# Kernel tuning notes

Hardware: AMD Instinct MI355X
Metric: run time of the kernel (lower is better)

## Reference

```python
import jax, jax.numpy as jnp
import numpy as np

SIGMA = 1.0  # RBF kernel bandwidth (init kwarg)

def setup_inputs() -> dict:
    key = jax.random.key(0)
    ks = jax.random.split(key, 5)
    B, N, D_in, D_emb = 8, 2048, 1024, 512
    scale = 1.0 / np.sqrt(D_in)
    return {
        "x": jax.random.normal(ks[0], (B, N, D_in), jnp.float32),
        "W_mu": jax.random.normal(ks[1], (D_emb, D_in), jnp.float32) * scale,
        "b_mu": jax.random.normal(ks[2], (D_emb,), jnp.float32) * scale,
        "W_logvar": jax.random.normal(ks[3], (D_emb, D_in), jnp.float32) * scale,
        "b_logvar": jax.random.normal(ks[4], (D_emb,), jnp.float32) * scale,
    }

def reference(x, W_mu, b_mu, W_logvar, b_logvar):
    # dual linear heads: (B,N,D_in) -> (B,N,D_emb)
    mu = jnp.einsum('bnd,ed->bne', x, W_mu) + b_mu
    logvar = jnp.einsum('bnd,ed->bne', x, W_logvar) + b_logvar
    sigma = jnp.exp(0.5 * logvar)
    # RBF kernel matrix K(x, x): (B,N,N) via ||xi||^2 + ||xj||^2 - 2 xi.xj
    sq = jnp.sum(x * x, axis=-1)                       # (B,N)
    gram = jnp.einsum('bnd,bmd->bnm', x, x)            # (B,N,N)
    dist = sq[:, :, None] + sq[:, None, :] - 2.0 * gram
    K = jnp.exp(-dist / (2.0 * SIGMA ** 2))            # (B,N,N)
    cov_diag = jnp.diagonal(K, axis1=1, axis2=2)       # (B,N) == exp(0) = 1
    sigma_adjusted = sigma * cov_diag[..., None]       # (B,N,D_emb)
    return (mu, sigma_adjusted)
```

## Files before the change

### kernel.cpp

```cpp
#include <hip/hip_runtime.h>
#include <hip/hip_bf16.h>
#include <math.h>

typedef __bf16 bf16;
typedef __attribute__((ext_vector_type(4))) float f32x4;
typedef __attribute__((ext_vector_type(4))) bf16 bf16x4;
typedef __attribute__((ext_vector_type(8))) bf16 bf16x8;

#define M_TOT 16384
#define K_TOT 1024
#define D_EMB 512
#define NT 32

__global__ __launch_bounds__(256) void cvt_w_img(
    const float* __restrict__ W_mu, const float* __restrict__ W_logvar,
    bf16* __restrict__ img)
{
    const int c  = blockIdx.x * 256 + threadIdx.x;
    const int l  = c & 63;
    const int kt = (c >> 6) & 31;
    const int es = c >> 11;
    const int col = es * 16 + (l & 15);
    const int k0  = kt * 32 + (l >> 4) * 8;
    const float* s = (col < D_EMB) ? (W_mu + (size_t)col * K_TOT + k0)
                                   : (W_logvar + (size_t)(col - D_EMB) * K_TOT + k0);
    f32x4 a = ((const f32x4*)s)[0];
    f32x4 b = ((const f32x4*)s)[1];
    bf16x8 o;
    o[0] = (bf16)a[0]; o[1] = (bf16)a[1]; o[2] = (bf16)a[2]; o[3] = (bf16)a[3];
    o[4] = (bf16)b[0]; o[5] = (bf16)b[1]; o[6] = (bf16)b[2]; o[7] = (bf16)b[3];
    *(bf16x8*)(img + (size_t)c * 8) = o;
}

__global__ __launch_bounds__(512, 1) void gpe_tall3(
    const float* __restrict__ x,
    const bf16* __restrict__ wimg,
    const float* __restrict__ b_mu,
    const float* __restrict__ b_logvar,
    float* __restrict__ out)
{
    __shared__ __align__(16) bf16 Alds[64 * 1024];

    const int tid  = threadIdx.x;
    const int lane = tid & 63;
    const int wc   = tid >> 6;
    const int fr   = lane & 15;
    const int g16  = lane >> 4;
    const int frx  = fr & 7;
    const int bm   = blockIdx.x;

    const int arow = tid >> 3;
    const int sl0  = tid & 7;
    const int rx   = arow & 7;
    const float* __restrict__ Asrc = x + (size_t)(bm * 64 + arow) * K_TOT;

    f32x4 stg[8];
    auto gload = [&](int c) {
#pragma unroll
        for (int j = 0; j < 4; ++j) {
            const int s = c * 32 + sl0 + 8 * j;
            stg[2 * j]     = *(const f32x4*)(Asrc + s * 8);
            stg[2 * j + 1] = *(const f32x4*)(Asrc + s * 8 + 4);
        }
    };
    auto cvtwrite = [&](int c) {
#pragma unroll
        for (int j = 0; j < 4; ++j) {
            const int s = c * 32 + sl0 + 8 * j;
            bf16x8 w;
#pragma unroll
            for (int q = 0; q < 4; ++q) {
                w[q]     = (bf16)stg[2 * j][q];
                w[q + 4] = (bf16)stg[2 * j + 1][q];
            }
            *(bf16x8*)&Alds[arow * 1024 + (s ^ rx) * 8] = w;
        }
    };

    const bf16* __restrict__ bl = wimg + lane * 8;
    bf16x8 bvA[4], bvB[4];
    auto loadB = [&](size_t e0, int t, bf16x8 (&bv)[4]) {
#pragma unroll
        for (int ns = 0; ns < 4; ++ns)
            bv[ns] = *(const bf16x8*)(bl + e0 + (size_t)ns * 16384 + t * 512);
    };

    f32x4 acc[4][4];
#pragma unroll
    for (int m = 0; m < 4; ++m)
#pragma unroll
        for (int n = 0; n < 4; ++n)
            acc[m][n] = (f32x4){0.f, 0.f, 0.f, 0.f};

    const size_t e0p0 = (size_t)(wc * 4) * 16384;
    const size_t e0p1 = (size_t)(32 + wc * 4) * 16384;

#define TILE_BODY(T, E0, BVC)                                                  \
    {                                                                          \
        const int t = (T);                                                     \
        bf16x8 afc[4];                                                         \
        _Pragma("unroll")                                                      \
        for (int m = 0; m < 4; ++m)                                            \
            afc[m] = *(const bf16x8*)&Alds[(m * 16 + fr) * 1024                \
                                           + ((t * 4 + g16) ^ frx) * 8];       \
        __builtin_amdgcn_s_setprio(1);                                         \
        _Pragma("unroll")                                                      \
        for (int ns = 0; ns < 4; ++ns)                                         \
            _Pragma("unroll")                                                  \
            for (int m = 0; m < 4; ++m)                                        \
                acc[m][ns] = __builtin_amdgcn_mfma_f32_16x16x32_bf16(          \
                    afc[m], BVC[ns], acc[m][ns], 0, 0, 0);                     \
        __builtin_amdgcn_s_setprio(0);                                         \
        if (t + 2 < NT) loadB(E0, t + 2, BVC);                                 \
    }

    gload(0);
    for (int c = 0; c < 4; ++c) {
        if (c == 0) asm volatile("s_waitcnt vmcnt(0)" ::: "memory");
        else        asm volatile("s_waitcnt vmcnt(8)" ::: "memory");
        cvtwrite(c);
        if (c < 3) gload(c + 1);
        if (c == 0) { loadB(e0p0, 0, bvA); loadB(e0p0, 1, bvB); }
        asm volatile("s_waitcnt lgkmcnt(0)" ::: "memory");
        __builtin_amdgcn_s_barrier();
#pragma unroll
        for (int tt = 0; tt < 8; tt += 2) {
            TILE_BODY(c * 8 + tt,     e0p0, bvA)
            TILE_BODY(c * 8 + tt + 1, e0p0, bvB)
        }
    }

    loadB(e0p1, 0, bvA);
    loadB(e0p1, 1, bvB);
    {
        float* __restrict__ obase = out;
#pragma unroll
        for (int m = 0; m < 4; ++m) {
            const int row0 = bm * 64 + m * 16 + g16 * 4;
#pragma unroll
            for (int ns = 0; ns < 4; ++ns) {
                const int cl = wc * 64 + ns * 16 + fr;
                const float bvs = b_mu[cl];
#pragma unroll
                for (int j = 0; j < 4; ++j)
                    obase[(size_t)(row0 + j) * D_EMB + cl] = acc[m][ns][j] + bvs;
            }
        }
    }

#pragma unroll
    for (int m = 0; m < 4; ++m)
#pragma unroll
        for (int n = 0; n < 4; ++n)
            acc[m][n] = (f32x4){0.f, 0.f, 0.f, 0.f};

#pragma unroll
    for (int tt = 0; tt < NT; tt += 2) {
        TILE_BODY(tt,     e0p1, bvA)
        TILE_BODY(tt + 1, e0p1, bvB)
    }
#undef TILE_BODY

    {
        float* __restrict__ obase = out + (size_t)M_TOT * D_EMB;
#pragma unroll
        for (int m = 0; m < 4; ++m) {
            const int row0 = bm * 64 + m * 16 + g16 * 4;
#pragma unroll
            for (int ns = 0; ns < 4; ++ns) {
                const int cl = wc * 64 + ns * 16 + fr;
                const float bvs = b_logvar[cl];
#pragma unroll
                for (int j = 0; j < 4; ++j)
                    obase[(size_t)(row0 + j) * D_EMB + cl] =
                        __expf(0.5f * (acc[m][ns][j] + bvs));
            }
        }
    }
}

#define LDS_STRIDE 40
__global__ __launch_bounds__(256) void gpe_gemm_fb(
    const float* __restrict__ x, const float* __restrict__ W_mu,
    const float* __restrict__ b_mu, const float* __restrict__ W_logvar,
    const float* __restrict__ b_logvar, float* __restrict__ out)
{
    __shared__ __align__(16) bf16 As[128][LDS_STRIDE];
    __shared__ __align__(16) bf16 Bs[128][LDS_STRIDE];
    const int tid = threadIdx.x, lane = tid & 63, wid = tid >> 6;
    const int wr = wid >> 1, wcn = wid & 1;
    const int bn = blockIdx.x & 7, bm = blockIdx.x >> 3;
    const int ebase = bn * 128;
    const bool is_mu = (ebase < D_EMB);
    const float* Wp = is_mu ? (W_mu + (size_t)ebase * K_TOT)
                            : (W_logvar + (size_t)(ebase - D_EMB) * K_TOT);
    const float* bias = is_mu ? b_mu : b_logvar;
    const int cbase = is_mu ? ebase : (ebase - D_EMB);
    float* obase = is_mu ? out : (out + (size_t)M_TOT * D_EMB);
    const float* Ap = x + (size_t)(bm * 128) * K_TOT;
    f32x4 acc[4][4];
#pragma unroll
    for (int m = 0; m < 4; ++m)
#pragma unroll
        for (int n = 0; n < 4; ++n) acc[m][n] = (f32x4){0.f, 0.f, 0.f, 0.f};
    const int fr = lane & 15, fk = (lane >> 4) * 8;
    const int arow = wr * 64 + fr, brow = wcn * 64 + fr;
    for (int kt = 0; kt < K_TOT / 32; ++kt) {
        const int k0 = kt * 32;
#pragma unroll
        for (int s = 0; s < 4; ++s) {
            const int idx = s * 256 + tid;
            const int row = idx >> 3, col = (idx & 7) << 2;
            f32x4 va = *reinterpret_cast<const f32x4*>(Ap + (size_t)row * K_TOT + k0 + col);
            f32x4 vb = *reinterpret_cast<const f32x4*>(Wp + (size_t)row * K_TOT + k0 + col);
            bf16x4 ha, hb;
#pragma unroll
            for (int j = 0; j < 4; ++j) { ha[j] = (bf16)va[j]; hb[j] = (bf16)vb[j]; }
            *reinterpret_cast<bf16x4*>(&As[row][col]) = ha;
            *reinterpret_cast<bf16x4*>(&Bs[row][col]) = hb;
        }
        __syncthreads();
        bf16x8 af[4], bfv[4];
#pragma unroll
        for (int m = 0; m < 4; ++m)
            af[m] = *reinterpret_cast<const bf16x8*>(&As[arow + m * 16][fk]);
#pragma unroll
        for (int n = 0; n < 4; ++n)
            bfv[n] = *reinterpret_cast<const bf16x8*>(&Bs[brow + n * 16][fk]);
#pragma unroll
        for (int m = 0; m < 4; ++m)
#pragma unroll
            for (int n = 0; n < 4; ++n)
                acc[m][n] = __builtin_amdgcn_mfma_f32_16x16x32_bf16(af[m], bfv[n], acc[m][n], 0, 0, 0);
        __syncthreads();
    }
#pragma unroll
    for (int m = 0; m < 4; ++m) {
        const int rbase = bm * 128 + wr * 64 + m * 16 + (lane >> 4) * 4;
#pragma unroll
        for (int n = 0; n < 4; ++n) {
            const int c = cbase + wcn * 64 + n * 16 + (lane & 15);
            const float bv = bias[c];
#pragma unroll
            for (int j = 0; j < 4; ++j) {
                float v = acc[m][n][j] + bv;
                if (!is_mu) v = __expf(0.5f * v);
                obase[(size_t)(rbase + j) * D_EMB + c] = v;
            }
        }
    }
}

extern "C" void kernel_launch(void* const* d_in, const int* in_sizes, int n_in,
                              void* d_out, int out_size, void* d_ws, size_t ws_size,
                              hipStream_t stream) {
    const float* x        = (const float*)d_in[0];
    const float* W_mu     = (const float*)d_in[1];
    const float* b_mu     = (const float*)d_in[2];
    const float* W_logvar = (const float*)d_in[3];
    const float* b_logvar = (const float*)d_in[4];
    float* out = (float*)d_out;

    const size_t ws_needed = (size_t)1024 * 1024 * sizeof(bf16);

    if (ws_size >= ws_needed) {
        bf16* wimg = (bf16*)d_ws;
        cvt_w_img<<<512, 256, 0, stream>>>(W_mu, W_logvar, wimg);
        gpe_tall3<<<256, 512, 0, stream>>>(x, wimg, b_mu, b_logvar, out);
    } else {
        gpe_gemm_fb<<<1024, 256, 0, stream>>>(x, W_mu, b_mu, W_logvar, b_logvar, out);
    }
}
```

Before: 48.58 us.

## Double workgroup to 16 waves, halve per-wave column tile, compute logvar pass first

The GEMM kernel now launches 1024 threads per block (16 waves), each covering 32 output columns instead of 64. That halves per-wave accumulators and B fragments and spreads the x staging loads over more threads. The order of the two output passes is swapped so the logvar/exp pass runs first and the mu pass last. This buys more latency hiding per CU, at the cost of reading each A fragment from LDS twice as often relative to the MFMAs and more barrier participants.

Result: slower. 80.84 us (+66.4%).

```diff
diff --git a/kernel.cpp b/kernel.cpp
--- a/kernel.cpp
+++ b/kernel.cpp
@@ -32,7 +32,7 @@
     *(bf16x8*)(img + (size_t)c * 8) = o;
 }
 
-__global__ __launch_bounds__(512, 1) void gpe_tall3(
+__global__ __launch_bounds__(1024, 1) void gpe_tall4(
     const float* __restrict__ x,
     const bf16* __restrict__ wimg,
     const float* __restrict__ b_mu,
@@ -43,57 +43,54 @@
 
     const int tid  = threadIdx.x;
     const int lane = tid & 63;
-    const int wc   = tid >> 6;
+    const int w    = tid >> 6;
     const int fr   = lane & 15;
     const int g16  = lane >> 4;
     const int frx  = fr & 7;
     const int bm   = blockIdx.x;
 
-    const int arow = tid >> 3;
-    const int sl0  = tid & 7;
+    const int arow = tid >> 4;
+    const int si   = tid & 15;
     const int rx   = arow & 7;
     const float* __restrict__ Asrc = x + (size_t)(bm * 64 + arow) * K_TOT;
 
-    f32x4 stg[8];
+    f32x4 stg[4];
     auto gload = [&](int c) {
 #pragma unroll
-        for (int j = 0; j < 4; ++j) {
-            const int s = c * 32 + sl0 + 8 * j;
-            stg[2 * j]     = *(const f32x4*)(Asrc + s * 8);
-            stg[2 * j + 1] = *(const f32x4*)(Asrc + s * 8 + 4);
-        }
+        for (int j = 0; j < 4; ++j)
+            stg[j] = *(const f32x4*)(Asrc + c * 256 + si * 16 + j * 4);
     };
     auto cvtwrite = [&](int c) {
 #pragma unroll
-        for (int j = 0; j < 4; ++j) {
-            const int s = c * 32 + sl0 + 8 * j;
-            bf16x8 w;
+        for (int h = 0; h < 2; ++h) {
+            bf16x8 wv;
 #pragma unroll
             for (int q = 0; q < 4; ++q) {
-                w[q]     = (bf16)stg[2 * j][q];
-                w[q + 4] = (bf16)stg[2 * j + 1][q];
-            }
-            *(bf16x8*)&Alds[arow * 1024 + (s ^ rx) * 8] = w;
+                wv[q]     = (bf16)stg[2 * h][q];
+                wv[q + 4] = (bf16)stg[2 * h + 1][q];
+            }
+            const int slot = c * 32 + si * 2 + h;
+            *(bf16x8*)&Alds[arow * 1024 + (slot ^ rx) * 8] = wv;
         }
     };
 
     const bf16* __restrict__ bl = wimg + lane * 8;
-    bf16x8 bvA[4], bvB[4];
-    auto loadB = [&](size_t e0, int t, bf16x8 (&bv)[4]) {
-#pragma unroll
-        for (int ns = 0; ns < 4; ++ns)
+    bf16x8 bvA[2], bvB[2];
+    auto loadB = [&](size_t e0, int t, bf16x8 (&bv)[2]) {
+#pragma unroll
+        for (int ns = 0; ns < 2; ++ns)
             bv[ns] = *(const bf16x8*)(bl + e0 + (size_t)ns * 16384 + t * 512);
     };
 
-    f32x4 acc[4][4];
+    f32x4 acc[4][2];
 #pragma unroll
     for (int m = 0; m < 4; ++m)
 #pragma unroll
-        for (int n = 0; n < 4; ++n)
+        for (int n = 0; n < 2; ++n)
             acc[m][n] = (f32x4){0.f, 0.f, 0.f, 0.f};
 
-    const size_t e0p0 = (size_t)(wc * 4) * 16384;
-    const size_t e0p1 = (size_t)(32 + wc * 4) * 16384;
+    const size_t e0p0 = (size_t)(32 + w * 2) * 16384;
+    const size_t e0p1 = (size_t)(w * 2) * 16384;
 
 #define TILE_BODY(T, E0, BVC)                                                  \
     {                                                                          \
@@ -105,7 +102,7 @@
                                            + ((t * 4 + g16) ^ frx) * 8];       \
         __builtin_amdgcn_s_setprio(1);                                         \
         _Pragma("unroll")                                                      \
-        for (int ns = 0; ns < 4; ++ns)                                         \
+        for (int ns = 0; ns < 2; ++ns)                                         \
             _Pragma("unroll")                                                  \
             for (int m = 0; m < 4; ++m)                                        \
                 acc[m][ns] = __builtin_amdgcn_mfma_f32_16x16x32_bf16(          \
@@ -117,7 +114,7 @@
     gload(0);
     for (int c = 0; c < 4; ++c) {
         if (c == 0) asm volatile("s_waitcnt vmcnt(0)" ::: "memory");
-        else        asm volatile("s_waitcnt vmcnt(8)" ::: "memory");
+        else        asm volatile("s_waitcnt vmcnt(4)" ::: "memory");
         cvtwrite(c);
         if (c < 3) gload(c + 1);
         if (c == 0) { loadB(e0p0, 0, bvA); loadB(e0p0, 1, bvB); }
@@ -133,17 +130,18 @@
     loadB(e0p1, 0, bvA);
     loadB(e0p1, 1, bvB);
     {
-        float* __restrict__ obase = out;
+        float* __restrict__ obase = out + (size_t)M_TOT * D_EMB;
 #pragma unroll
         for (int m = 0; m < 4; ++m) {
             const int row0 = bm * 64 + m * 16 + g16 * 4;
 #pragma unroll
-            for (int ns = 0; ns < 4; ++ns) {
-                const int cl = wc * 64 + ns * 16 + fr;
-                const float bvs = b_mu[cl];
+            for (int ns = 0; ns < 2; ++ns) {
+                const int cl = w * 32 + ns * 16 + fr;
+                const float bvs = b_logvar[cl];
 #pragma unroll
                 for (int j = 0; j < 4; ++j)
-                    obase[(size_t)(row0 + j) * D_EMB + cl] = acc[m][ns][j] + bvs;
+                    obase[(size_t)(row0 + j) * D_EMB + cl] =
+                        __expf(0.5f * (acc[m][ns][j] + bvs));
             }
         }
     }
@@ -151,7 +149,7 @@
 #pragma unroll
     for (int m = 0; m < 4; ++m)
 #pragma unroll
-        for (int n = 0; n < 4; ++n)
+        for (int n = 0; n < 2; ++n)
             acc[m][n] = (f32x4){0.f, 0.f, 0.f, 0.f};
 
 #pragma unroll
@@ -162,18 +160,17 @@
 #undef TILE_BODY
 
     {
-        float* __restrict__ obase = out + (size_t)M_TOT * D_EMB;
+        float* __restrict__ obase = out;
 #pragma unroll
         for (int m = 0; m < 4; ++m) {
             const int row0 = bm * 64 + m * 16 + g16 * 4;
 #pragma unroll
-            for (int ns = 0; ns < 4; ++ns) {
-                const int cl = wc * 64 + ns * 16 + fr;
-                const float bvs = b_logvar[cl];
+            for (int ns = 0; ns < 2; ++ns) {
+                const int cl = w * 32 + ns * 16 + fr;
+                const float bvs = b_mu[cl];
 #pragma unroll
                 for (int j = 0; j < 4; ++j)
-                    obase[(size_t)(row0 + j) * D_EMB + cl] =
-                        __expf(0.5f * (acc[m][ns][j] + bvs));
+                    obase[(size_t)(row0 + j) * D_EMB + cl] = acc[m][ns][j] + bvs;
             }
         }
     }
@@ -266,7 +263,7 @@
     if (ws_size >= ws_needed) {
         bf16* wimg = (bf16*)d_ws;
         cvt_w_img<<<512, 256, 0, stream>>>(W_mu, W_logvar, wimg);
-        gpe_tall3<<<256, 512, 0, stream>>>(x, wimg, b_mu, b_logvar, out);
+        gpe_tall4<<<256, 1024, 0, stream>>>(x, wimg, b_mu, b_logvar, out);
     } else {
         gpe_gemm_fb<<<1024, 256, 0, stream>>>(x, W_mu, b_mu, W_logvar, b_logvar, out);
     }
```
